# Kernel optimization log

Measured on AMD Instinct MI355X. Metric: run time of the kernel, lower is better.

Reference implementation:

```python
import jax, jax.numpy as jnp
import numpy as np

N = 50000      # nodes
E = 800000     # edges (before self-loops)
H = 6          # heads
F_IN = 64
F_OUT = 64
NEG_SLOPE = 0.2  # PyG GATv2Conv default


def setup_inputs() -> dict:
    key = jax.random.key(0)
    k1, k2, k3, k4, k5 = jax.random.split(key, 5)
    x = jax.random.normal(k1, (N, F_IN), jnp.float32)
    edge_idx = jax.random.randint(k2, (2, E), 0, N, dtype=jnp.int64)
    scale = 1.0 / np.sqrt(F_IN)
    W_l = jax.random.normal(k3, (F_IN, H * F_OUT), jnp.float32) * scale
    W_r = jax.random.normal(k4, (F_IN, H * F_OUT), jnp.float32) * scale
    att = jax.random.normal(k5, (H, F_OUT), jnp.float32) * scale
    bias = jnp.zeros((F_OUT,), jnp.float32)
    return {"x": x, "edge_idx": edge_idx, "W_l": W_l, "W_r": W_r, "att": att, "bias": bias}


def reference(x, edge_idx, W_l, W_r, att, bias):
    n = x.shape[0]
    # PyG GATv2Conv adds self-loops by default
    loops = jnp.arange(n, dtype=edge_idx.dtype)
    src = jnp.concatenate([edge_idx[0], loops])  # message sources j
    dst = jnp.concatenate([edge_idx[1], loops])  # message targets i

    gl = (x @ W_l).reshape(n, H, F_OUT)  # x_l (source-side projection)
    gr = (x @ W_r).reshape(n, H, F_OUT)  # x_r (target-side projection)

    # attention logits: a^T LeakyReLU(x_l[j] + x_r[i])  -> [Et, H]
    s = jax.nn.leaky_relu(gl[src] + gr[dst], NEG_SLOPE)
    e = jnp.einsum('ehf,hf->eh', s, att)

    # segment softmax over incoming edges of each destination node
    m = jax.ops.segment_max(e, dst, num_segments=n)          # [N, H]
    p = jnp.exp(e - m[dst])                                  # [Et, H]
    denom = jax.ops.segment_sum(p, dst, num_segments=n)     # [N, H]
    alpha = p / (denom[dst] + 1e-16)

    # weighted scatter-add of source messages
    msg = alpha[:, :, None] * gl[src]                        # [Et, H, F]
    out = jax.ops.segment_sum(msg, dst, num_segments=n)     # [N, H, F]

    # concat=False -> mean over heads, then bias, then SELU
    out = out.mean(axis=1) + bias
    return jax.nn.selu(out)
```

## Files before the change

### kernel.cpp

```cpp
#include <hip/hip_runtime.h>
#include <hip/hip_bf16.h>
#include <hip/hip_fp16.h>

typedef _Float16 half8 __attribute__((ext_vector_type(8)));
typedef _Float16 half4_t __attribute__((ext_vector_type(4)));
typedef _Float16 h2 __attribute__((ext_vector_type(2)));
typedef float f32x4 __attribute__((ext_vector_type(4)));
typedef unsigned int u32;

#define NEG_SLOPE 0.2f
#define SELU_SCALE 1.0507009873554805f
#define SELU_ALPHA 1.6732632423543772f
#define LOG2E 1.4426950408889634f

#if __has_builtin(__builtin_amdgcn_fdot2)
#define FDOT2(a, b, c) __builtin_amdgcn_fdot2((a), (b), (c), false)
#else
static __device__ inline float FDOT2(h2 a, h2 b, float c) {
    return c + (float)a[0] * (float)b[0] + (float)a[1] * (float)b[1];
}
#endif

static __device__ inline h2 h2max(h2 a, h2 b) {
#if __has_builtin(__builtin_elementwise_max)
    return __builtin_elementwise_max(a, b);
#else
    h2 r; r[0] = a[0] > b[0] ? a[0] : b[0]; r[1] = a[1] > b[1] ? a[1] : b[1]; return r;
#endif
}

static __device__ inline h2 shfl_h2(h2 v, int d) {
    u32 u = __builtin_bit_cast(u32, v);
    return __builtin_bit_cast(h2, (u32)__shfl_xor((int)u, d, 64));
}

static __device__ inline float fexp2(float x) {
    float r;
    asm("v_exp_f32 %0, %1" : "=v"(r) : "v"(x));
    return r;
}

static __device__ inline h2 pk2(float a) {
#if __has_builtin(__builtin_amdgcn_cvt_pkrtz)
    return __builtin_bit_cast(h2, __builtin_amdgcn_cvt_pkrtz(a, a));
#else
    _Float16 h = (_Float16)a; return (h2){h, h};
#endif
}

__global__ __launch_bounds__(256) void gemm_kernel(
    const float* __restrict__ x, const float* __restrict__ Wl,
    const float* __restrict__ Wr, _Float16* __restrict__ glr, int n_nodes)
{
    __shared__ float xs[64 * 68];
    int row0 = blockIdx.x * 64;
    if (row0 >= n_nodes) return;

    {
        int t = threadIdx.x;
        #pragma unroll
        for (int i = 0; i < 4; i++) {
            int idx = t + i * 256;
            int r = idx >> 4, c = (idx & 15) * 4;
            int row = row0 + r;
            f32x4 v = (f32x4){0.f, 0.f, 0.f, 0.f};
            if (row < n_nodes) v = *(const f32x4*)(x + (size_t)row * 64 + c);
            *(f32x4*)(xs + r * 68 + c) = v;
        }
    }
    __syncthreads();

    int wid  = threadIdx.x >> 6;
    int lane = threadIdx.x & 63;
    int l15  = lane & 15;
    int g    = lane >> 4;
    int kb   = g * 8;
    int colbase = wid * 192;

    half8 bw0[12], bw1[12];
    #pragma unroll
    for (int t = 0; t < 12; t++) {
        int col = colbase + t * 16 + l15;
        const float* wcol = (col < 384) ? (Wl + col) : (Wr + (col - 384));
        #pragma unroll
        for (int j = 0; j < 8; j++) {
            bw0[t][j] = (_Float16)wcol[(size_t)(kb + j) * 384];
            bw1[t][j] = (_Float16)wcol[(size_t)(32 + kb + j) * 384];
        }
    }

    #pragma unroll
    for (int rt = 0; rt < 4; rt++) {
        int r0 = rt * 16;
        half8 a0, a1;
        #pragma unroll
        for (int j = 0; j < 8; j++) {
            a0[j] = (_Float16)xs[(r0 + l15) * 68 + kb + j];
            a1[j] = (_Float16)xs[(r0 + l15) * 68 + 32 + kb + j];
        }
        int nodeRow = row0 + r0 + l15;
        #pragma unroll
        for (int t = 0; t < 12; t++) {
            f32x4 acc = (f32x4){0.f, 0.f, 0.f, 0.f};
            acc = __builtin_amdgcn_mfma_f32_16x16x32_f16(bw0[t], a0, acc, 0, 0, 0);
            acc = __builtin_amdgcn_mfma_f32_16x16x32_f16(bw1[t], a1, acc, 0, 0, 0);
            if (nodeRow < n_nodes) {
                int c0 = colbase + t * 16 + g * 4;
                half4_t hv;
                #pragma unroll
                for (int r = 0; r < 4; r++) hv[r] = (_Float16)acc[r];
                *(half4_t*)(glr + (size_t)nodeRow * 768 + c0) = hv;
            }
        }
    }
}

__global__ void hist_kernel(const int* __restrict__ eidx, int* count, int n_edges) {
    int i = blockIdx.x * blockDim.x + threadIdx.x;
    if (i < n_edges) atomicAdd(&count[eidx[n_edges + i]], 1);
}

__global__ __launch_bounds__(256) void scan_local_kernel(
    const int* __restrict__ count, int* __restrict__ row_ptr,
    int* __restrict__ blksum, int n)
{
    __shared__ int ws[4];
    int blk = blockIdx.x, t = threadIdx.x;
    int base = blk * 1024 + t * 4;
    int a0 = (base + 0 < n) ? count[base + 0] + 1 : 0;
    int a1 = (base + 1 < n) ? count[base + 1] + 1 : 0;
    int a2 = (base + 2 < n) ? count[base + 2] + 1 : 0;
    int a3 = (base + 3 < n) ? count[base + 3] + 1 : 0;
    int tsum = a0 + a1 + a2 + a3;
    int lane = t & 63, wid = t >> 6;
    int s = tsum;
    #pragma unroll
    for (int d = 1; d < 64; d <<= 1) {
        int u = __shfl_up(s, d, 64);
        if (lane >= d) s += u;
    }
    if (lane == 63) ws[wid] = s;
    __syncthreads();
    int woff = 0;
    #pragma unroll
    for (int w = 0; w < 4; w++) if (w < wid) woff += ws[w];
    int excl = woff + s - tsum;
    if (base + 0 < n) row_ptr[base + 0] = excl;
    if (base + 1 < n) row_ptr[base + 1] = excl + a0;
    if (base + 2 < n) row_ptr[base + 2] = excl + a0 + a1;
    if (base + 3 < n) row_ptr[base + 3] = excl + a0 + a1 + a2;
    if (t == 255) blksum[blk] = woff + s;
}

__global__ __launch_bounds__(64) void scan_blk_kernel(
    int* __restrict__ blksum, int* __restrict__ row_ptr, int nblk, int n)
{
    int lane = threadIdx.x;
    int v = (lane < nblk) ? blksum[lane] : 0;
    int s = v;
    #pragma unroll
    for (int d = 1; d < 64; d <<= 1) {
        int u = __shfl_up(s, d, 64);
        if (lane >= d) s += u;
    }
    if (lane < nblk) blksum[lane] = s - v;
    if (lane == 63) row_ptr[n] = s;
}

__global__ void cursor_kernel(int* __restrict__ row_ptr,
                              const int* __restrict__ blksum,
                              int* __restrict__ cursor,
                              int* __restrict__ sorted_src, int n) {
    int i = blockIdx.x * blockDim.x + threadIdx.x;
    if (i < n) {
        int rp = row_ptr[i] + blksum[i >> 10];
        row_ptr[i] = rp;
        cursor[i] = rp + 1;
        sorted_src[rp] = i;
    }
}

__global__ void scatter_kernel(const int* __restrict__ eidx, int* cursor,
                               int* sorted_src, int n_edges) {
    int i = blockIdx.x * blockDim.x + threadIdx.x;
    if (i < n_edges) {
        int d = eidx[n_edges + i];
        int s = eidx[i];
        int pos = atomicAdd(&cursor[d], 1);
        sorted_src[pos] = s;
    }
}

__global__ __launch_bounds__(256) void edge_kernel(
    const _Float16* __restrict__ glr,
    const int* __restrict__ row_ptr,
    const int* __restrict__ sorted_src,
    const float* __restrict__ att,
    const float* __restrict__ bias,
    float* __restrict__ out, int n_nodes)
{
    int wid  = threadIdx.x >> 6;
    int lane = threadIdx.x & 63;
    int gwid = blockIdx.x * 4 + wid;
    int GW   = gridDim.x * 4;
    int g   = lane >> 4;
    int l0  = lane & 15;
    int oct = l0 >> 3;
    int q   = l0 & 7;
    u32 l16 = (u32)l0 * 16u;

    const char* glr_b = (const char*)glr;
    const _Float16 c02 = (_Float16)NEG_SLOPE;

    h2 att_h[12];
    #pragma unroll
    for (int P = 0; P < 3; P++) {
        int h = 2 * P + oct;
        f32x4 av0 = *(const f32x4*)(att + h * 64 + q * 8);
        f32x4 av1 = *(const f32x4*)(att + h * 64 + q * 8 + 4);
        att_h[P * 4 + 0] = (h2){(_Float16)(av0[0] * LOG2E), (_Float16)(av0[1] * LOG2E)};
        att_h[P * 4 + 1] = (h2){(_Float16)(av0[2] * LOG2E), (_Float16)(av0[3] * LOG2E)};
        att_h[P * 4 + 2] = (h2){(_Float16)(av1[0] * LOG2E), (_Float16)(av1[1] * LOG2E)};
        att_h[P * 4 + 3] = (h2){(_Float16)(av1[2] * LOG2E), (_Float16)(av1[3] * LOG2E)};
    }

    for (int node = gwid; node < n_nodes; node += GW) {
        h2 gr_h[12];
        {
            u32 rbase = (u32)node * 1536u + 768u;
            #pragma unroll
            for (int P = 0; P < 3; P++) {
                half8 gv = *(const half8*)(glr_b + rbase + (u32)P * 256u + l16);
                gr_h[P * 4 + 0] = ((h2*)&gv)[0];
                gr_h[P * 4 + 1] = ((h2*)&gv)[1];
                gr_h[P * 4 + 2] = ((h2*)&gv)[2];
                gr_h[P * 4 + 3] = ((h2*)&gv)[3];
            }
        }

        float m[3], sden[3];
        h2 acc[12];
        #pragma unroll
        for (int P = 0; P < 3; P++) { m[P] = -1e30f; sden[P] = 0.f; }
        #pragma unroll
        for (int j = 0; j < 12; j++) acc[j] = (h2){(_Float16)0.f, (_Float16)0.f};

        int rp = row_ptr[node], re = row_ptr[node + 1];
        int reclamp = re - 1;

        auto lsrc = [&](int idx) {
            int ii = idx < reclamp ? idx : reclamp;
            return sorted_src[ii];
        };

        half8 A0, A1, A2, B0, B1, B2;

#define LOADX(X0, X1, X2, S)                                                 \
        {                                                                    \
            u32 o = (u32)(S) * 1536u + l16;                                  \
            X0 = *(const half8*)(glr_b + o);                                 \
            X1 = *(const half8*)(glr_b + o + 256);                           \
            X2 = *(const half8*)(glr_b + o + 512);                           \
        }

#define PROC(X0, X1, X2, BASE)                                               \
        {                                                                    \
            bool active = ((BASE) + g) < re;                                 \
            float e[3];                                                      \
            _Pragma("unroll")                                                \
            for (int P = 0; P < 3; P++) {                                    \
                h2 t0 = ((h2*)&X0)[0], t1 = ((h2*)&X0)[1],                   \
                   t2 = ((h2*)&X0)[2], t3 = ((h2*)&X0)[3];                   \
                if (P == 1) { t0 = ((h2*)&X1)[0]; t1 = ((h2*)&X1)[1];        \
                              t2 = ((h2*)&X1)[2]; t3 = ((h2*)&X1)[3]; }      \
                if (P == 2) { t0 = ((h2*)&X2)[0]; t1 = ((h2*)&X2)[1];        \
                              t2 = ((h2*)&X2)[2]; t3 = ((h2*)&X2)[3]; }      \
                t0 = t0 + gr_h[P * 4 + 0]; t1 = t1 + gr_h[P * 4 + 1];        \
                t2 = t2 + gr_h[P * 4 + 2]; t3 = t3 + gr_h[P * 4 + 3];        \
                t0 = h2max(t0, t0 * c02); t1 = h2max(t1, t1 * c02);          \
                t2 = h2max(t2, t2 * c02); t3 = h2max(t3, t3 * c02);          \
                e[P] = FDOT2(t3, att_h[P * 4 + 3], FDOT2(t2, att_h[P * 4 + 2],\
                       FDOT2(t1, att_h[P * 4 + 1], FDOT2(t0, att_h[P * 4 + 0],\
                       0.f))));                                              \
            }                                                                \
            _Pragma("unroll")                                                \
            for (int d = 1; d < 8; d <<= 1) {                                \
                e[0] += __shfl_xor(e[0], d, 64);                             \
                e[1] += __shfl_xor(e[1], d, 64);                             \
                e[2] += __shfl_xor(e[2], d, 64);                             \
            }                                                                \
            if (active) {                                                    \
                _Pragma("unroll")                                            \
                for (int P = 0; P < 3; P++) {                                \
                    float mo = m[P];                                         \
                    float mn = fmaxf(mo, e[P]);                              \
                    float r  = fexp2(mo - mn);                               \
                    float p  = fexp2(e[P] - mn);                             \
                    m[P] = mn;                                               \
                    sden[P] = sden[P] * r + p;                               \
                    h2 r2 = pk2(r), p2 = pk2(p);                             \
                    const h2* xv = (P == 0) ? (const h2*)&X0                 \
                                 : (P == 1) ? (const h2*)&X1 : (const h2*)&X2;\
                    acc[P * 4 + 0] = acc[P * 4 + 0] * r2 + p2 * xv[0];       \
                    acc[P * 4 + 1] = acc[P * 4 + 1] * r2 + p2 * xv[1];       \
                    acc[P * 4 + 2] = acc[P * 4 + 2] * r2 + p2 * xv[2];       \
                    acc[P * 4 + 3] = acc[P * 4 + 3] * r2 + p2 * xv[3];       \
                }                                                            \
            }                                                                \
        }

        {
            LOADX(A0, A1, A2, lsrc(rp + g));
            int sN = lsrc(rp + 4 + g);
            int base = rp;
            for (;;) {
                LOADX(B0, B1, B2, sN);
                int sN2 = lsrc(base + 8 + g);
                PROC(A0, A1, A2, base);
                base += 4; if (base >= re) break;
                LOADX(A0, A1, A2, sN2);
                sN = lsrc(base + 8 + g);
                PROC(B0, B1, B2, base);
                base += 4; if (base >= re) break;
            }
        }
#undef PROC
#undef LOADX

        #pragma unroll
        for (int d = 16; d < 64; d <<= 1) {
            #pragma unroll
            for (int P = 0; P < 3; P++) {
                float mo = __shfl_xor(m[P], d, 64);
                float so = __shfl_xor(sden[P], d, 64);
                h2 ao0 = shfl_h2(acc[P * 4 + 0], d);
                h2 ao1 = shfl_h2(acc[P * 4 + 1], d);
                h2 ao2 = shfl_h2(acc[P * 4 + 2], d);
                h2 ao3 = shfl_h2(acc[P * 4 + 3], d);
                float mn = fmaxf(m[P], mo);
                float ra = exp2f(m[P] - mn);
                float rb = exp2f(mo - mn);
                sden[P] = sden[P] * ra + so * rb;
                h2 ra2 = pk2(ra), rb2 = pk2(rb);
                acc[P * 4 + 0] = acc[P * 4 + 0] * ra2 + ao0 * rb2;
                acc[P * 4 + 1] = acc[P * 4 + 1] * ra2 + ao1 * rb2;
                acc[P * 4 + 2] = acc[P * 4 + 2] * ra2 + ao2 * rb2;
                acc[P * 4 + 3] = acc[P * 4 + 3] * ra2 + ao3 * rb2;
                m[P] = mn;
            }
        }

        h2 iv[3];
        #pragma unroll
        for (int P = 0; P < 3; P++) {
            float inv = 1.0f / (sden[P] + 1e-16f);
            _Float16 ih = (_Float16)inv;
            iv[P] = (h2){ih, ih};
        }
        float of[8];
        #pragma unroll
        for (int j = 0; j < 4; j++) {
            h2 o = acc[0 * 4 + j] * iv[0] + acc[1 * 4 + j] * iv[1] + acc[2 * 4 + j] * iv[2];
            o = o + shfl_h2(o, 8);
            of[2 * j]     = (float)o[0];
            of[2 * j + 1] = (float)o[1];
        }

        if (lane < 8) {
            f32x4 b0 = *(const f32x4*)(bias + q * 8);
            f32x4 b1 = *(const f32x4*)(bias + q * 8 + 4);
            f32x4 ov0, ov1;
            #pragma unroll
            for (int k = 0; k < 4; k++) {
                float v0 = of[k] * (1.0f / 6.0f) + b0[k];
                float v1 = of[k + 4] * (1.0f / 6.0f) + b1[k];
                ov0[k] = (v0 > 0.f) ? SELU_SCALE * v0
                                    : SELU_SCALE * SELU_ALPHA * (__expf(v0) - 1.0f);
                ov1[k] = (v1 > 0.f) ? SELU_SCALE * v1
                                    : SELU_SCALE * SELU_ALPHA * (__expf(v1) - 1.0f);
            }
            float* op = out + (size_t)node * 64 + q * 8;
            *(f32x4*)op = ov0;
            *(f32x4*)(op + 4) = ov1;
        }
    }
}

extern "C" void kernel_launch(void* const* d_in, const int* in_sizes, int n_in,
                              void* d_out, int out_size, void* d_ws, size_t ws_size,
                              hipStream_t stream) {
    const float* x    = (const float*)d_in[0];
    const int*   eidx = (const int*)d_in[1];
    const float* Wl   = (const float*)d_in[2];
    const float* Wr   = (const float*)d_in[3];
    const float* att  = (const float*)d_in[4];
    const float* bias = (const float*)d_in[5];
    float* out = (float*)d_out;

    int n = in_sizes[0] / 64;
    int E = in_sizes[1] / 2;
    int Et = E + n;

    char* w = (char*)d_ws;
    size_t off = 0;
    auto carve = [&](size_t bytes) {
        void* p = w + off;
        off = (off + bytes + 255) & ~(size_t)255;
        return p;
    };
    _Float16* glr   = (_Float16*)carve((size_t)n * 768 * sizeof(_Float16));
    int* count      = (int*)carve((size_t)n * sizeof(int));
    int* row_ptr    = (int*)carve((size_t)(n + 1) * sizeof(int));
    int* cursor     = (int*)carve((size_t)n * sizeof(int));
    int* sorted_src = (int*)carve((size_t)Et * sizeof(int));
    int* blksum     = (int*)carve(64 * sizeof(int));
    (void)ws_size;

    int nb_n = (n + 255) / 256;
    int nb_e = (E + 255) / 256;
    int nblk = (n + 1023) / 1024;

    hipMemsetAsync(count, 0, (size_t)n * sizeof(int), stream);
    hipLaunchKernelGGL(hist_kernel, dim3(nb_e), dim3(256), 0, stream, eidx, count, E);
    hipLaunchKernelGGL(scan_local_kernel, dim3(nblk), dim3(256), 0, stream,
                       count, row_ptr, blksum, n);
    hipLaunchKernelGGL(scan_blk_kernel, dim3(1), dim3(64), 0, stream,
                       blksum, row_ptr, nblk, n);
    hipLaunchKernelGGL(cursor_kernel, dim3(nb_n), dim3(256), 0, stream,
                       row_ptr, blksum, cursor, sorted_src, n);
    hipLaunchKernelGGL(scatter_kernel, dim3(nb_e), dim3(256), 0, stream,
                       eidx, cursor, sorted_src, E);
    hipLaunchKernelGGL(gemm_kernel, dim3((n + 63) / 64), dim3(256), 0, stream,
                       x, Wl, Wr, glr, n);
    hipLaunchKernelGGL(edge_kernel, dim3(2048), dim3(256), 0, stream,
                       glr, row_ptr, sorted_src, att, bias, out, n);
}
```

Before: 244.6 us.

## Split gl/gr projections into separate arrays and use atomic work queue for nodes

Splits the interleaved gl|gr fp16 projection buffer into two separate arrays, so the gathered source rows (gl) sit in a dense 768-byte-stride table. Edge gathers then touch a more compact footprint, which should improve L2/MALL hit rates. It also replaces the static grid-stride node assignment with a per-wave atomic counter for dynamic load balancing across uneven node degrees. The cost is one extra memset plus one global atomic per node processed.

```diff
diff --git a/kernel.cpp b/kernel.cpp
--- a/kernel.cpp
+++ b/kernel.cpp
@@ -50,7 +50,8 @@
 
 __global__ __launch_bounds__(256) void gemm_kernel(
     const float* __restrict__ x, const float* __restrict__ Wl,
-    const float* __restrict__ Wr, _Float16* __restrict__ glr, int n_nodes)
+    const float* __restrict__ Wr, _Float16* __restrict__ glA,
+    _Float16* __restrict__ glB, int n_nodes)
 {
     __shared__ float xs[64 * 68];
     int row0 = blockIdx.x * 64;
@@ -109,7 +110,10 @@
                 half4_t hv;
                 #pragma unroll
                 for (int r = 0; r < 4; r++) hv[r] = (_Float16)acc[r];
-                *(half4_t*)(glr + (size_t)nodeRow * 768 + c0) = hv;
+                _Float16* dst = (c0 < 384)
+                    ? (glA + (size_t)nodeRow * 384 + c0)
+                    : (glB + (size_t)nodeRow * 384 + (c0 - 384));
+                *(half4_t*)dst = hv;
             }
         }
     }
@@ -192,24 +196,24 @@
 }
 
 __global__ __launch_bounds__(256) void edge_kernel(
-    const _Float16* __restrict__ glr,
+    const _Float16* __restrict__ glA,
+    const _Float16* __restrict__ glB,
     const int* __restrict__ row_ptr,
     const int* __restrict__ sorted_src,
     const float* __restrict__ att,
     const float* __restrict__ bias,
-    float* __restrict__ out, int n_nodes)
+    float* __restrict__ out,
+    int* __restrict__ wq, int n_nodes)
 {
-    int wid  = threadIdx.x >> 6;
     int lane = threadIdx.x & 63;
-    int gwid = blockIdx.x * 4 + wid;
-    int GW   = gridDim.x * 4;
     int g   = lane >> 4;
     int l0  = lane & 15;
     int oct = l0 >> 3;
     int q   = l0 & 7;
     u32 l16 = (u32)l0 * 16u;
 
-    const char* glr_b = (const char*)glr;
+    const char* glA_b = (const char*)glA;
+    const char* glB_b = (const char*)glB;
     const _Float16 c02 = (_Float16)NEG_SLOPE;
 
     h2 att_h[12];
@@ -224,13 +228,18 @@
         att_h[P * 4 + 3] = (h2){(_Float16)(av1[2] * LOG2E), (_Float16)(av1[3] * LOG2E)};
     }
 
-    for (int node = gwid; node < n_nodes; node += GW) {
+    for (;;) {
+        int node;
+        if (lane == 0) node = atomicAdd(wq, 1);
+        node = __shfl(node, 0, 64);
+        if (node >= n_nodes) break;
+
         h2 gr_h[12];
         {
-            u32 rbase = (u32)node * 1536u + 768u;
+            u32 rbase = (u32)node * 768u;
             #pragma unroll
             for (int P = 0; P < 3; P++) {
-                half8 gv = *(const half8*)(glr_b + rbase + (u32)P * 256u + l16);
+                half8 gv = *(const half8*)(glB_b + rbase + (u32)P * 256u + l16);
                 gr_h[P * 4 + 0] = ((h2*)&gv)[0];
                 gr_h[P * 4 + 1] = ((h2*)&gv)[1];
                 gr_h[P * 4 + 2] = ((h2*)&gv)[2];
@@ -257,10 +266,10 @@
 
 #define LOADX(X0, X1, X2, S)                                                 \
         {                                                                    \
-            u32 o = (u32)(S) * 1536u + l16;                                  \
-            X0 = *(const half8*)(glr_b + o);                                 \
-            X1 = *(const half8*)(glr_b + o + 256);                           \
-            X2 = *(const half8*)(glr_b + o + 512);                           \
+            u32 o = (u32)(S) * 768u + l16;                                   \
+            X0 = *(const half8*)(glA_b + o);                                 \
+            X1 = *(const half8*)(glA_b + o + 256);                           \
+            X2 = *(const half8*)(glA_b + o + 512);                           \
         }
 
 #define PROC(X0, X1, X2, BASE)                                               \
@@ -408,12 +417,14 @@
         off = (off + bytes + 255) & ~(size_t)255;
         return p;
     };
-    _Float16* glr   = (_Float16*)carve((size_t)n * 768 * sizeof(_Float16));
+    _Float16* glA   = (_Float16*)carve((size_t)n * 384 * sizeof(_Float16));
+    _Float16* glB   = (_Float16*)carve((size_t)n * 384 * sizeof(_Float16));
     int* count      = (int*)carve((size_t)n * sizeof(int));
     int* row_ptr    = (int*)carve((size_t)(n + 1) * sizeof(int));
     int* cursor     = (int*)carve((size_t)n * sizeof(int));
     int* sorted_src = (int*)carve((size_t)Et * sizeof(int));
     int* blksum     = (int*)carve(64 * sizeof(int));
+    int* wq         = (int*)carve(4 * sizeof(int));
     (void)ws_size;
 
     int nb_n = (n + 255) / 256;
@@ -421,6 +432,7 @@
     int nblk = (n + 1023) / 1024;
 
     hipMemsetAsync(count, 0, (size_t)n * sizeof(int), stream);
+    hipMemsetAsync(wq, 0, 4 * sizeof(int), stream);
     hipLaunchKernelGGL(hist_kernel, dim3(nb_e), dim3(256), 0, stream, eidx, count, E);
     hipLaunchKernelGGL(scan_local_kernel, dim3(nblk), dim3(256), 0, stream,
                        count, row_ptr, blksum, n);
@@ -431,7 +443,7 @@
     hipLaunchKernelGGL(scatter_kernel, dim3(nb_e), dim3(256), 0, stream,
                        eidx, cursor, sorted_src, E);
     hipLaunchKernelGGL(gemm_kernel, dim3((n + 63) / 64), dim3(256), 0, stream,
-                       x, Wl, Wr, glr, n);
+                       x, Wl, Wr, glA, glB, n);
     hipLaunchKernelGGL(edge_kernel, dim3(2048), dim3(256), 0, stream,
-                       glr, row_ptr, sorted_src, att, bias, out, n);
-}
+                       glA, glB, row_ptr, sorted_src, att, bias, out, wq, n);
+}
```

Result: slower. 823.6 us (+236.7%).
